# Optimization experiments

Measured on AMD Instinct MI355X. Metric: run time of the kernel, lower is better.

The kernel has to match this reference:

```python
import jax, jax.numpy as jnp
import numpy as np

B, C, H, W = 2, 64, 128, 128
K, SCALE, NUM_RES = 3, 2, 2
KK = K * K


def conv(x, w, b, pad=0):
    y = jax.lax.conv_general_dilated(x, w, (1, 1), [(pad, pad), (pad, pad)],
                                     dimension_numbers=('NCHW', 'OIHW', 'NCHW'))
    return y + b[None, :, None, None]


def unfold_dilated(x, k, d):
    # mimics nn.Unfold(kernel_size=k, dilation=d, padding=(k//2)*d) -> (b, c, k*k, h, w)
    pad = (k // 2) * d
    b, c, h, w = x.shape
    xp = jnp.pad(x, ((0, 0), (0, 0), (pad, pad), (pad, pad)))
    slices = [xp[:, :, i * d:i * d + h, j * d:j * d + w]
              for i in range(k) for j in range(k)]
    return jnp.stack(slices, axis=2)


def setup_inputs() -> dict:
    key = jax.random.key(0)
    ks = jax.random.split(key, 32)
    def p(k, shape, s=0.05):
        return jax.random.normal(k, shape, dtype=jnp.float32) * s
    H2, W2 = H * SCALE, W * SCALE
    return {
        'depth':  p(ks[0], (B, C, H2, W2), 1.0),
        'guide':  p(ks[1], (B, C, H2, W2), 1.0),
        'inputs': p(ks[2], (B, C, H, W), 1.0),
        # depth_kernel branch: 1x1 C->C (ReLU), 1x1 C->k^2
        'dk_w1': p(ks[3], (C, C, 1, 1)), 'dk_b1': jnp.zeros((C,), jnp.float32),
        'dk_w2': p(ks[4], (KK, C, 1, 1)), 'dk_b2': jnp.zeros((KK,), jnp.float32),
        # guide_kernel branch
        'gk_w1': p(ks[5], (C, C, 1, 1)), 'gk_b1': jnp.zeros((C,), jnp.float32),
        'gk_w2': p(ks[6], (KK, C, 1, 1)), 'gk_b2': jnp.zeros((KK,), jnp.float32),
        # weight_net: 3x3 2C->C (ReLU), 3x3 C->C (ReLU, TUnet stand-in), 3x3 C->1
        'wn_w1': p(ks[7], (C, 2 * C, 3, 3)), 'wn_b1': jnp.zeros((C,), jnp.float32),
        'wn_w2': p(ks[8], (C, C, 3, 3)), 'wn_b2': jnp.zeros((C,), jnp.float32),
        'wn_w3': p(ks[9], (1, C, 3, 3)), 'wn_b3': jnp.zeros((1,), jnp.float32),
        # residual blocks on inputs: NUM_RES x (conv3x3-ReLU-conv3x3 + skip)
        'rb_w': p(ks[10], (NUM_RES, 2, C, C, 3, 3)),
        'rb_b': jnp.zeros((NUM_RES, 2, C), jnp.float32),
        'aff_scale': 0.5 * KK * jnp.ones((1,), jnp.float32),
    }


def reference(depth, guide, inputs,
              dk_w1, dk_b1, dk_w2, dk_b2,
              gk_w1, gk_b1, gk_w2, gk_b2,
              wn_w1, wn_b1, wn_w2, wn_b2, wn_w3, wn_b3,
              rb_w, rb_b, aff_scale):
    # weight map
    wm = jax.nn.relu(conv(jnp.concatenate([depth, guide], axis=1), wn_w1, wn_b1, 1))
    wm = jax.nn.relu(conv(wm, wn_w2, wn_b2, 1))
    weight_map = conv(wm, wn_w3, wn_b3, 1)                       # (b,1,h_,w_)
    # per-pixel kernels
    dk = conv(jax.nn.relu(conv(depth, dk_w1, dk_b1)), dk_w2, dk_b2)
    gk = conv(jax.nn.relu(conv(guide, gk_w1, gk_b1)), gk_w2, gk_b2)
    dk = jax.nn.softmax(dk, axis=1)
    gk = jax.nn.softmax(gk, axis=1)
    fuse = weight_map * dk + (1.0 - weight_map) * gk
    fuse = jnp.tanh(fuse) / (aff_scale + 1e-8)
    ksum = jnp.maximum(jnp.sum(jnp.abs(fuse), axis=1, keepdims=True) + 1e-4, 1.0)
    fuse = fuse / ksum                                            # (b,k^2,h_,w_)
    # residual conv stack on low-res inputs
    x = inputs
    for i in range(NUM_RES):
        r = jax.nn.relu(conv(x, rb_w[i, 0], rb_b[i, 0], 1))
        r = conv(r, rb_w[i, 1], rb_b[i, 1], 1)
        x = x + r
    b, c, h, w = x.shape
    up = jax.image.resize(x, (b, c, h * SCALE, w * SCALE), method='bilinear')
    unf = unfold_dilated(up, K, SCALE)                            # (b,c,k^2,h_,w_)
    out = jnp.einsum('bkhw,bckhw->bchw', fuse, unf)
    return out
```

## Files before the change

### kernel.cpp

```cpp
#include <hip/hip_runtime.h>
#include <hip/hip_bf16.h>
#include <math.h>

#define HW2 (256*256)
#define HW1 (128*128)

typedef __attribute__((ext_vector_type(8))) short short8;
typedef __attribute__((ext_vector_type(4))) float floatx4;

__device__ __forceinline__ float b2f(ushort u) {
    union { unsigned int i; float f; } v; v.i = ((unsigned int)u) << 16; return v.f;
}
__device__ __forceinline__ ushort f2b(float f) {
    __hip_bfloat16 h = __float2bfloat16(f); return *(ushort*)&h;
}
__device__ __forceinline__ void pin(const short8& v) {
    asm volatile("" :: "v"(v));
}
__device__ __forceinline__ float fast_tanh(float x) {
    float cx = fminf(fmaxf(x, -15.f), 15.f);
    float t = __expf(2.f * cx);
    return (t - 1.f) / (t + 1.f);
}

__global__ __launch_bounds__(256)
void repack_all(const float* __restrict__ wn_w1, const float* __restrict__ wn_w2,
                const float* __restrict__ rb_w,
                const float* __restrict__ dk_w1, const float* __restrict__ gk_w1,
                const float* __restrict__ dk_w2, const float* __restrict__ gk_w2,
                const float* __restrict__ wn_w3,
                ushort* __restrict__ wt_wn1, ushort* __restrict__ wt_wn2,
                ushort* __restrict__ wt_rb,
                ushort* __restrict__ w1d, ushort* __restrict__ w1g,
                ushort* __restrict__ w2d, ushort* __restrict__ w2g,
                ushort* __restrict__ wt3) {
    int idx = blockIdx.x * 256 + threadIdx.x;
    int role = blockIdx.y;
    if (role == 0) {
        if (idx >= 73728) return;
        int o = idx / 1152; int rem = idx - o * 1152;
        int ci = rem / 9;   int t = rem - ci * 9;
        wt_wn1[(((size_t)(ci >> 5) * 9 + t) * 64 + o) * 32 + (ci & 31)] = f2b(wn_w1[idx]);
    } else if (role <= 5) {
        if (idx >= 36864) return;
        const float* w = (role == 1) ? wn_w2 : rb_w + (size_t)(role - 2) * 36864;
        ushort* wt     = (role == 1) ? wt_wn2 : wt_rb + (size_t)(role - 2) * 36864;
        int o = idx / 576; int rem = idx - o * 576;
        int ci = rem / 9;  int t = rem - ci * 9;
        wt[(((size_t)(ci >> 5) * 9 + t) * 64 + o) * 32 + (ci & 31)] = f2b(w[idx]);
    } else if (role == 6) {
        if (idx >= 10240) return;
        if (idx < 4096)      w1d[idx] = f2b(dk_w1[idx]);
        else if (idx < 8192) w1g[idx - 4096] = f2b(gk_w1[idx - 4096]);
        else if (idx < 9216) { int i = idx - 8192; w2d[i] = (i >> 6) < 9 ? f2b(dk_w2[i]) : (ushort)0; }
        else                 { int i = idx - 9216; w2g[i] = (i >> 6) < 9 ? f2b(gk_w2[i]) : (ushort)0; }
    } else {
        if (idx >= 9216) return;
        int kc = idx / 512; int rem = idx - kc * 512;
        int n = rem >> 5, c = rem & 31;
        int cc = kc / 9, t = kc - cc * 9;
        wt3[idx] = (n == 0) ? f2b(wn_w3[(cc * 32 + c) * 9 + t]) : (ushort)0;
    }
}

__global__ __launch_bounds__(256)
void to_chunked(const float* __restrict__ in, ushort* __restrict__ outc,
                int H, int W, int Cchunks) {
    int P = W + 2, Q = H + 2;
    int plane_px = P * Q;
    int idx = blockIdx.x * 256 + threadIdx.x;
    if (idx >= plane_px) return;
    int py = idx / P, px = idx - py * P;
    int bc = blockIdx.y;
    int b = bc / Cchunks, cc = bc - b * Cchunks;
    ushort* dst = outc + ((size_t)bc * plane_px + idx) * 32;
    if (py == 0 || py == Q - 1 || px == 0 || px == P - 1) {
        for (int c = 0; c < 32; ++c) dst[c] = 0;
        return;
    }
    int y = py - 1, x = px - 1;
    const float* src = in + ((size_t)b * (Cchunks * 32) + cc * 32) * H * W
                          + (size_t)y * W + x;
    for (int c = 0; c < 32; ++c)
        dst[c] = f2b(src[(size_t)c * H * W]);
}

__global__ __launch_bounds__(256)
void to_chunked_hi(const float* __restrict__ depth, const float* __restrict__ guide,
                   ushort* __restrict__ outc) {
    const int P = 258;
    int plane_px = P * P;
    int idx = blockIdx.x * 256 + threadIdx.x;
    if (idx >= plane_px) return;
    int py = idx / P, px = idx - py * P;
    int pl = blockIdx.y;
    const float* srcb = (pl < 4) ? depth : guide;
    int bc = pl & 3;
    int b = bc >> 1, cc = bc & 1;
    ushort* dst = outc + ((size_t)pl * plane_px + idx) * 32;
    if (py == 0 || py == P - 1 || px == 0 || px == P - 1) {
        for (int c = 0; c < 32; ++c) dst[c] = 0;
        return;
    }
    int y = py - 1, x = px - 1;
    const float* src = srcb + ((size_t)b * 64 + cc * 32) * HW2 + (size_t)y * 256 + x;
    for (int c = 0; c < 32; ++c)
        dst[c] = f2b(src[(size_t)c * HW2]);
}

__global__ __launch_bounds__(256)
void zero_border2(ushort* __restrict__ buf256, ushort* __restrict__ buf128) {
    int region = blockIdx.y;
    int H = region ? 128 : 256;
    int P = H + 2, Q = H + 2;
    ushort* buf = region ? buf128 : buf256;
    int nb = 2 * P + 2 * H;
    int idx = blockIdx.x * 256 + threadIdx.x;
    if (idx >= nb * 8) return;
    int pl = idx / nb, r = idx - pl * nb;
    int py, px;
    if (r < P)          { py = 0;     px = r; }
    else if (r < 2 * P) { py = Q - 1; px = r - P; }
    else { int k = r - 2 * P; py = 1 + (k >> 1); px = (k & 1) ? P - 1 : 0; }
    ushort* dst = buf + ((size_t)pl * P * Q + (size_t)py * P + px) * 32;
    for (int c = 0; c < 32; ++c) dst[c] = 0;
}

template<int NCHUNK, int ROWS, bool RELU, bool HAS_SKIP, bool CONCAT2>
__global__ __launch_bounds__(256)
void conv3x3_reg(const ushort* __restrict__ inA, const ushort* __restrict__ inB,
                 const ushort* __restrict__ wt, const float* __restrict__ bias,
                 const ushort* __restrict__ skip, ushort* __restrict__ outc,
                 int H, int W) {
    const int P = W + 2;
    const size_t plane = (size_t)P * (H + 2) * 32;
    int tid = threadIdx.x;
    int wv = tid >> 6, lane = tid & 63, ml = lane & 15, q = lane >> 4;
    int x0 = blockIdx.x * 16;
    int rowsPerBlock = (blockDim.x >> 6) * ROWS;
    int yb = blockIdx.y * rowsPerBlock + wv * ROWS;
    int b = blockIdx.z;

    floatx4 acc[ROWS][4];
#pragma unroll
    for (int r = 0; r < ROWS; ++r)
#pragma unroll
        for (int n = 0; n < 4; ++n) acc[r][n] = (floatx4){0.f, 0.f, 0.f, 0.f};

    for (int cc = 0; cc < NCHUNK; ++cc) {
        const ushort* base;
        if (CONCAT2) {
            constexpr int HC = NCHUNK / 2;
            if (cc < HC) base = inA + ((size_t)(b * HC + cc)) * plane;
            else         base = inB + ((size_t)(b * HC + cc - HC)) * plane;
        } else {
            base = inA + ((size_t)(b * NCHUNK + cc)) * plane;
        }
        const ushort* wb = wt + (size_t)cc * 18432;
#pragma unroll
        for (int t = 0; t < 9; ++t) {
            int dy = t / 3, dx = t - 3 * dy;
            short8 afr[ROWS], bfr[4];
#pragma unroll
            for (int r = 0; r < ROWS; ++r)
                afr[r] = *(const short8*)&base[((size_t)(yb + r + dy) * P
                                               + (x0 + ml + dx)) * 32 + q * 8];
#pragma unroll
            for (int n = 0; n < 4; ++n)
                bfr[n] = *(const short8*)&wb[(size_t)(t * 64 + n * 16 + ml) * 32 + q * 8];
#pragma unroll
            for (int r = 0; r < ROWS; ++r)
#pragma unroll
                for (int n = 0; n < 4; ++n)
                    acc[r][n] = __builtin_amdgcn_mfma_f32_16x16x32_bf16(
                        afr[r], bfr[n], acc[r][n], 0, 0, 0);
        }
    }

#pragma unroll
    for (int r = 0; r < ROWS; ++r) {
        int y = yb + r;
#pragma unroll
        for (int n = 0; n < 4; ++n) {
            int ch = n * 16 + ml;
            int occ = ch >> 5, ocl = ch & 31;
            float bs = bias[ch];
            size_t pbase = ((size_t)(b * 2 + occ)) * plane + ((size_t)(y + 1) * P) * 32 + ocl;
#pragma unroll
            for (int e = 0; e < 4; ++e) {
                int x = x0 + q * 4 + e;
                float v = acc[r][n][e] + bs;
                if (RELU) v = fmaxf(v, 0.f);
                if (HAS_SKIP)
                    v += b2f(skip[((size_t)(b * 2 + occ)) * plane
                                  + ((size_t)(y + 1) * P + (x + 1)) * 32 + ocl]);
                outc[pbase + (size_t)(x + 1) * 32] = f2b(v);
            }
        }
    }
}

__global__ __launch_bounds__(256, 2)
void kernels_fuse_mfma(const ushort* __restrict__ depth_c, const ushort* __restrict__ guide_c,
                       const ushort* __restrict__ bufB,
                       const ushort* __restrict__ wt3, const float* __restrict__ wn_b3,
                       const ushort* __restrict__ w1d, const float* __restrict__ b1d,
                       const ushort* __restrict__ w2d, const float* __restrict__ b2d,
                       const ushort* __restrict__ w1g, const float* __restrict__ b1g,
                       const ushort* __restrict__ w2g, const float* __restrict__ b2g,
                       const float* __restrict__ aff, float* __restrict__ fuse_out) {
    __shared__ __align__(16) ushort hid[2][4][16 * 72];
    __shared__ float wmv[4][16];

    int tid = threadIdx.x;
    int wv = tid >> 6, lane = tid & 63, ml = lane & 15, q = lane >> 4;
    int p0 = blockIdx.x * 64 + wv * 16;
    int b = p0 >> 16, rem0 = p0 & 65535;
    const size_t plane = (size_t)258 * 258 * 32;

    int rem = rem0 + ml;
    int y = rem >> 8, x = rem & 255;
    size_t poff = ((size_t)(y + 1) * 258 + (x + 1)) * 32;

    short8 afr[2][2];
#pragma unroll
    for (int kc = 0; kc < 2; ++kc) {
        afr[0][kc] = *(const short8*)&depth_c[(size_t)(b * 2 + kc) * plane + poff + q * 8];
        afr[1][kc] = *(const short8*)&guide_c[(size_t)(b * 2 + kc) * plane + poff + q * 8];
    }
    const ushort* bb0 = bufB + (size_t)(b * 2 + 0) * plane;
    const ushort* bb1 = bufB + (size_t)(b * 2 + 1) * plane;
    short8 a30[9], a31[9];
#pragma unroll
    for (int t = 0; t < 9; ++t) {
        int dy = t / 3, dx = t - 3 * dy;
        size_t o = ((size_t)(y + dy) * 258 + (x + dx)) * 32 + q * 8;
        a30[t] = *(const short8*)&bb0[o];
        a31[t] = *(const short8*)&bb1[o];
    }

    pin(afr[0][0]); pin(afr[0][1]); pin(afr[1][0]); pin(afr[1][1]);

    floatx4 acc[2][4];
#pragma unroll
    for (int br = 0; br < 2; ++br)
#pragma unroll
        for (int nt = 0; nt < 4; ++nt) acc[br][nt] = (floatx4){0.f, 0.f, 0.f, 0.f};
#pragma unroll
    for (int nt = 0; nt < 4; ++nt)
#pragma unroll
        for (int kc = 0; kc < 2; ++kc) {
            short8 bD = *(const short8*)&w1d[(size_t)((nt * 16 + ml) * 64 + kc * 32 + q * 8)];
            short8 bG = *(const short8*)&w1g[(size_t)((nt * 16 + ml) * 64 + kc * 32 + q * 8)];
            acc[0][nt] = __builtin_amdgcn_mfma_f32_16x16x32_bf16(afr[0][kc], bD, acc[0][nt], 0, 0, 0);
            acc[1][nt] = __builtin_amdgcn_mfma_f32_16x16x32_bf16(afr[1][kc], bG, acc[1][nt], 0, 0, 0);
        }

#pragma unroll
    for (int t = 0; t < 9; ++t) pin(a30[t]);
    floatx4 dw[4];
#pragma unroll
    for (int u = 0; u < 4; ++u) dw[u] = (floatx4){0.f, 0.f, 0.f, 0.f};
#pragma unroll
    for (int t = 0; t < 9; ++t) {
        short8 b3 = *(const short8*)&wt3[(size_t)(t * 512 + ml * 32 + q * 8)];
        dw[t & 3] = __builtin_amdgcn_mfma_f32_16x16x32_bf16(a30[t], b3, dw[t & 3], 0, 0, 0);
    }
#pragma unroll
    for (int t = 0; t < 9; ++t) pin(a31[t]);
#pragma unroll
    for (int t = 0; t < 9; ++t) {
        short8 b3 = *(const short8*)&wt3[(size_t)((9 + t) * 512 + ml * 32 + q * 8)];
        dw[t & 3] = __builtin_amdgcn_mfma_f32_16x16x32_bf16(a31[t], b3, dw[t & 3], 0, 0, 0);
    }
    floatx4 dwm = (dw[0] + dw[1]) + (dw[2] + dw[3]);
    if (ml == 0) {
#pragma unroll
        for (int e = 0; e < 4; ++e) wmv[wv][q * 4 + e] = dwm[e];
    }

#pragma unroll
    for (int br = 0; br < 2; ++br) {
        const float* b1 = br ? b1g : b1d;
        ushort* h = hid[br][wv];
#pragma unroll
        for (int nt = 0; nt < 4; ++nt) {
            float bs = b1[nt * 16 + ml];
#pragma unroll
            for (int e = 0; e < 4; ++e) {
                float v = acc[br][nt][e] + bs;
                v = fmaxf(v, 0.f);
                h[(q * 4 + e) * 72 + nt * 16 + ml] = f2b(v);
            }
        }
    }

    floatx4 d2[2];
    d2[0] = (floatx4){0.f, 0.f, 0.f, 0.f};
    d2[1] = (floatx4){0.f, 0.f, 0.f, 0.f};
#pragma unroll
    for (int kc = 0; kc < 2; ++kc) {
        short8 a2d = *(const short8*)&w2d[(size_t)(ml * 64 + kc * 32 + q * 8)];
        short8 a2g = *(const short8*)&w2g[(size_t)(ml * 64 + kc * 32 + q * 8)];
        short8 hfd = *(const short8*)&hid[0][wv][ml * 72 + kc * 32 + q * 8];
        short8 hfg = *(const short8*)&hid[1][wv][ml * 72 + kc * 32 + q * 8];
        d2[0] = __builtin_amdgcn_mfma_f32_16x16x32_bf16(a2d, hfd, d2[0], 0, 0, 0);
        d2[1] = __builtin_amdgcn_mfma_f32_16x16x32_bf16(a2g, hfg, d2[1], 0, 0, 0);
    }

    float wm = wmv[wv][ml] + wn_b3[0];

    float sm[2][4];
#pragma unroll
    for (int br = 0; br < 2; ++br) {
        const float* b2 = br ? b2g : b2d;
        float lg[4];
#pragma unroll
        for (int e = 0; e < 4; ++e) {
            int j = q * 4 + e;
            lg[e] = (j < 9) ? (d2[br][e] + b2[j]) : -1e30f;
        }
        float m = fmaxf(fmaxf(lg[0], lg[1]), fmaxf(lg[2], lg[3]));
        m = fmaxf(m, __shfl_xor(m, 16));
        m = fmaxf(m, __shfl_xor(m, 32));
        float s = 0.f;
#pragma unroll
        for (int e = 0; e < 4; ++e) { lg[e] = __expf(lg[e] - m); s += lg[e]; }
        s += __shfl_xor(s, 16);
        s += __shfl_xor(s, 32);
        float inv = 1.f / s;
#pragma unroll
        for (int e = 0; e < 4; ++e) sm[br][e] = lg[e] * inv;
    }

    float inv_av = 1.f / (aff[0] + 1e-8f);
    float f[4];
    float s = 0.f;
#pragma unroll
    for (int e = 0; e < 4; ++e) {
        float v = wm * sm[0][e] + (1.f - wm) * sm[1][e];
        v = fast_tanh(v) * inv_av;
        f[e] = v;
        s += fabsf(v);
    }
    s += __shfl_xor(s, 16);
    s += __shfl_xor(s, 32);
    float ksum = s + 1e-4f;
    if (ksum < 1.f) ksum = 1.f;
    float invk = 1.f / ksum;
#pragma unroll
    for (int e = 0; e < 4; ++e) {
        int j = q * 4 + e;
        if (j < 9)
            fuse_out[((size_t)b * 9 + j) * HW2 + rem0 + ml] = f[e] * invk;
    }
}

__global__ __launch_bounds__(256)
void fuse_apply_up(const float* __restrict__ fuse, const ushort* __restrict__ r2c,
                   float* __restrict__ out) {
    int p = blockIdx.x * 256 + threadIdx.x;
    int pl = blockIdx.y;
    int b = pl >> 1, cc = pl & 1;
    int y = p >> 8, x = p & 255;

    int my = y >> 1, mx = x >> 1;
    float wyA = (y & 1) ? 0.75f : 0.25f;  float wyB = 1.f - wyA;
    float wxA = (x & 1) ? 0.75f : 0.25f;  float wxB = 1.f - wxA;
    int R0y = my + ((y & 1) ? 0 : -1) - 1;
    int R0x = mx + ((x & 1) ? 0 : -1) - 1;

    const float* f = fuse + (size_t)b * 9 * HW2 + p;
    float coef[4][4];
#pragma unroll
    for (int k = 0; k < 4; ++k)
#pragma unroll
        for (int l = 0; l < 4; ++l) coef[k][l] = 0.f;

#pragma unroll
    for (int ty = 0; ty < 3; ++ty) {
        int yp = y + (ty - 1) * 2;
        if (yp < 0 || yp > 255) continue;
#pragma unroll
        for (int tx = 0; tx < 3; ++tx) {
            int xp = x + (tx - 1) * 2;
            if (xp < 0 || xp > 255) continue;
            float fv = f[(size_t)(ty * 3 + tx) * HW2];
            coef[ty][tx]         += fv * wyA * wxA;
            coef[ty][tx + 1]     += fv * wyA * wxB;
            coef[ty + 1][tx]     += fv * wyB * wxA;
            coef[ty + 1][tx + 1] += fv * wyB * wxB;
        }
    }

    const ushort* base = r2c + (size_t)pl * 130 * 130 * 32;
    float acc[32];
#pragma unroll
    for (int c = 0; c < 32; ++c) acc[c] = 0.f;
#pragma unroll
    for (int k = 0; k < 4; ++k) {
        int ry = R0y + k; ry = ry < 0 ? 0 : (ry > 127 ? 127 : ry);
#pragma unroll
        for (int l = 0; l < 4; ++l) {
            int rx = R0x + l; rx = rx < 0 ? 0 : (rx > 127 ? 127 : rx);
            float cf = coef[k][l];
            const ushort* u = base + ((size_t)(ry + 1) * 130 + (rx + 1)) * 32;
#pragma unroll
            for (int c = 0; c < 32; ++c) acc[c] = fmaf(cf, b2f(u[c]), acc[c]);
        }
    }
    float* ob = out + ((size_t)(b * 64 + cc * 32)) * HW2 + p;
#pragma unroll
    for (int c = 0; c < 32; ++c) ob[(size_t)c * HW2] = acc[c];
}

extern "C" void kernel_launch(void* const* d_in, const int* in_sizes, int n_in,
                              void* d_out, int out_size, void* d_ws, size_t ws_size,
                              hipStream_t stream) {
    const float* depth  = (const float*)d_in[0];
    const float* guide  = (const float*)d_in[1];
    const float* inputs = (const float*)d_in[2];
    const float* dk_w1  = (const float*)d_in[3];
    const float* dk_b1  = (const float*)d_in[4];
    const float* dk_w2  = (const float*)d_in[5];
    const float* dk_b2  = (const float*)d_in[6];
    const float* gk_w1  = (const float*)d_in[7];
    const float* gk_b1  = (const float*)d_in[8];
    const float* gk_w2  = (const float*)d_in[9];
    const float* gk_b2  = (const float*)d_in[10];
    const float* wn_w1  = (const float*)d_in[11];
    const float* wn_b1  = (const float*)d_in[12];
    const float* wn_w2  = (const float*)d_in[13];
    const float* wn_b2  = (const float*)d_in[14];
    const float* wn_w3  = (const float*)d_in[15];
    const float* wn_b3  = (const float*)d_in[16];
    const float* rb_w   = (const float*)d_in[17];
    const float* rb_b   = (const float*)d_in[18];
    const float* aff    = (const float*)d_in[19];
    float* out = (float*)d_out;

    float* ws = (float*)d_ws;
    size_t off = 0;
    const size_t CH256 = 4260096;
    const size_t CH128 = 1081600;
    ushort* depth_c = (ushort*)(ws + off); off += CH256;
    ushort* guide_c = (ushort*)(ws + off); off += CH256;
    ushort* bufA    = (ushort*)(ws + off); off += CH256;
    ushort* bufB    = (ushort*)(ws + off); off += CH256;
    ushort* inp_c   = (ushort*)(ws + off); off += CH128;
    ushort* r0      = (ushort*)(ws + off); off += CH128;
    ushort* r1      = (ushort*)(ws + off); off += CH128;
    ushort* r2      = (ushort*)(ws + off); off += CH128;
    float* fuse     = ws + off; off += 1179648;
    ushort* wt_wn1  = (ushort*)(ws + off); off += 36864;
    ushort* wt_wn2  = (ushort*)(ws + off); off += 18432;
    ushort* wt_rb   = (ushort*)(ws + off); off += 73728;
    ushort* w1d_b   = (ushort*)(ws + off); off += 2048;
    ushort* w1g_b   = (ushort*)(ws + off); off += 2048;
    ushort* w2d_b   = (ushort*)(ws + off); off += 512;
    ushort* w2g_b   = (ushort*)(ws + off); off += 512;
    ushort* wt3_b   = (ushort*)(ws + off); off += 4608;

    repack_all<<<dim3(288, 8), 256, 0, stream>>>(
        wn_w1, wn_w2, rb_w, dk_w1, gk_w1, dk_w2, gk_w2, wn_w3,
        wt_wn1, wt_wn2, wt_rb, w1d_b, w1g_b, w2d_b, w2g_b, wt3_b);

    to_chunked_hi<<<dim3(261, 8), 256, 0, stream>>>(depth, guide, depth_c);
    to_chunked<<<dim3(67, 4), 256, 0, stream>>>(inputs, inp_c, 128, 128, 2);

    zero_border2<<<dim3(33, 2), 256, 0, stream>>>(bufA, r0);

    conv3x3_reg<4, 4, true, false, true ><<<dim3(16, 16, 2), 256, 0, stream>>>(
        depth_c, guide_c, wt_wn1, wn_b1, nullptr, bufA, 256, 256);
    conv3x3_reg<2, 4, true, false, false><<<dim3(16, 16, 2), 256, 0, stream>>>(
        bufA, nullptr, wt_wn2, wn_b2, nullptr, bufB, 256, 256);

    kernels_fuse_mfma<<<2048, 256, 0, stream>>>(depth_c, guide_c, bufB,
                                                wt3_b, wn_b3,
                                                w1d_b, dk_b1, w2d_b, dk_b2,
                                                w1g_b, gk_b1, w2g_b, gk_b2,
                                                aff, fuse);

    conv3x3_reg<2, 2, true,  false, false><<<dim3(8, 16, 2), 256, 0, stream>>>(
        inp_c, nullptr, wt_rb + 0 * 36864, rb_b + 0 * 64, nullptr, r0, 128, 128);
    conv3x3_reg<2, 2, false, true,  false><<<dim3(8, 16, 2), 256, 0, stream>>>(
        r0, nullptr, wt_rb + 1 * 36864, rb_b + 1 * 64, inp_c, r1, 128, 128);
    conv3x3_reg<2, 2, true,  false, false><<<dim3(8, 16, 2), 256, 0, stream>>>(
        r1, nullptr, wt_rb + 2 * 36864, rb_b + 2 * 64, nullptr, r0, 128, 128);
    conv3x3_reg<2, 2, false, true,  false><<<dim3(8, 16, 2), 256, 0, stream>>>(
        r0, nullptr, wt_rb + 3 * 36864, rb_b + 3 * 64, r1, r2, 128, 128);

    fuse_apply_up<<<dim3(256, 4), 256, 0, stream>>>(fuse, r2, out);
}
```

Measured before the change: 334.9 us.

## Vectorize layout-conversion stores, batch conv loads per kernel row, drop register pins

The layout-conversion and border-zeroing kernels now write each pixel's 32 bf16 channels as four 16-byte vector stores instead of 32 scalar stores. The 3x3 conv loop is restructured to issue all A and B fragment loads for one kernel row (three taps) before the MFMAs, so more loads are in flight. The conv kernel also gets a launch-bounds occupancy hint of 2. The asm pin barriers in the fused kernel are removed, leaving load scheduling to the compiler. The trade-off is higher register pressure in the conv kernel and loss of the hand-forced load ordering.

```diff
diff --git a/kernel.cpp b/kernel.cpp
--- a/kernel.cpp
+++ b/kernel.cpp
@@ -13,9 +13,6 @@
 }
 __device__ __forceinline__ ushort f2b(float f) {
     __hip_bfloat16 h = __float2bfloat16(f); return *(ushort*)&h;
-}
-__device__ __forceinline__ void pin(const short8& v) {
-    asm volatile("" :: "v"(v));
 }
 __device__ __forceinline__ float fast_tanh(float x) {
     float cx = fminf(fmaxf(x, -15.f), 15.f);
@@ -74,15 +71,21 @@
     int bc = blockIdx.y;
     int b = bc / Cchunks, cc = bc - b * Cchunks;
     ushort* dst = outc + ((size_t)bc * plane_px + idx) * 32;
+    short8* d8 = (short8*)dst;
     if (py == 0 || py == Q - 1 || px == 0 || px == P - 1) {
-        for (int c = 0; c < 32; ++c) dst[c] = 0;
+        short8 z = (short8){0, 0, 0, 0, 0, 0, 0, 0};
+        d8[0] = z; d8[1] = z; d8[2] = z; d8[3] = z;
         return;
     }
     int y = py - 1, x = px - 1;
     const float* src = in + ((size_t)b * (Cchunks * 32) + cc * 32) * H * W
                           + (size_t)y * W + x;
+    ushort tmp[32];
+#pragma unroll
     for (int c = 0; c < 32; ++c)
-        dst[c] = f2b(src[(size_t)c * H * W]);
+        tmp[c] = f2b(src[(size_t)c * H * W]);
+#pragma unroll
+    for (int v = 0; v < 4; ++v) d8[v] = *(short8*)&tmp[v * 8];
 }
 
 __global__ __launch_bounds__(256)
@@ -98,14 +101,20 @@
     int bc = pl & 3;
     int b = bc >> 1, cc = bc & 1;
     ushort* dst = outc + ((size_t)pl * plane_px + idx) * 32;
+    short8* d8 = (short8*)dst;
     if (py == 0 || py == P - 1 || px == 0 || px == P - 1) {
-        for (int c = 0; c < 32; ++c) dst[c] = 0;
+        short8 z = (short8){0, 0, 0, 0, 0, 0, 0, 0};
+        d8[0] = z; d8[1] = z; d8[2] = z; d8[3] = z;
         return;
     }
     int y = py - 1, x = px - 1;
     const float* src = srcb + ((size_t)b * 64 + cc * 32) * HW2 + (size_t)y * 256 + x;
+    ushort tmp[32];
+#pragma unroll
     for (int c = 0; c < 32; ++c)
-        dst[c] = f2b(src[(size_t)c * HW2]);
+        tmp[c] = f2b(src[(size_t)c * HW2]);
+#pragma unroll
+    for (int v = 0; v < 4; ++v) d8[v] = *(short8*)&tmp[v * 8];
 }
 
 __global__ __launch_bounds__(256)
@@ -123,11 +132,13 @@
     else if (r < 2 * P) { py = Q - 1; px = r - P; }
     else { int k = r - 2 * P; py = 1 + (k >> 1); px = (k & 1) ? P - 1 : 0; }
     ushort* dst = buf + ((size_t)pl * P * Q + (size_t)py * P + px) * 32;
-    for (int c = 0; c < 32; ++c) dst[c] = 0;
+    short8 z = (short8){0, 0, 0, 0, 0, 0, 0, 0};
+    short8* d8 = (short8*)dst;
+    d8[0] = z; d8[1] = z; d8[2] = z; d8[3] = z;
 }
 
 template<int NCHUNK, int ROWS, bool RELU, bool HAS_SKIP, bool CONCAT2>
-__global__ __launch_bounds__(256)
+__global__ __launch_bounds__(256, 2)
 void conv3x3_reg(const ushort* __restrict__ inA, const ushort* __restrict__ inB,
                  const ushort* __restrict__ wt, const float* __restrict__ bias,
                  const ushort* __restrict__ skip, ushort* __restrict__ outc,
@@ -158,22 +169,27 @@
         }
         const ushort* wb = wt + (size_t)cc * 18432;
 #pragma unroll
-        for (int t = 0; t < 9; ++t) {
-            int dy = t / 3, dx = t - 3 * dy;
-            short8 afr[ROWS], bfr[4];
-#pragma unroll
-            for (int r = 0; r < ROWS; ++r)
-                afr[r] = *(const short8*)&base[((size_t)(yb + r + dy) * P
-                                               + (x0 + ml + dx)) * 32 + q * 8];
-#pragma unroll
-            for (int n = 0; n < 4; ++n)
-                bfr[n] = *(const short8*)&wb[(size_t)(t * 64 + n * 16 + ml) * 32 + q * 8];
-#pragma unroll
-            for (int r = 0; r < ROWS; ++r)
+        for (int dy = 0; dy < 3; ++dy) {
+            short8 afr[3][ROWS], bfr[3][4];
+#pragma unroll
+            for (int dx = 0; dx < 3; ++dx) {
+#pragma unroll
+                for (int r = 0; r < ROWS; ++r)
+                    afr[dx][r] = *(const short8*)&base[((size_t)(yb + r + dy) * P
+                                                       + (x0 + ml + dx)) * 32 + q * 8];
 #pragma unroll
                 for (int n = 0; n < 4; ++n)
-                    acc[r][n] = __builtin_amdgcn_mfma_f32_16x16x32_bf16(
-                        afr[r], bfr[n], acc[r][n], 0, 0, 0);
+                    bfr[dx][n] = *(const short8*)&wb[(size_t)((dy * 3 + dx) * 64
+                                                              + n * 16 + ml) * 32 + q * 8];
+            }
+#pragma unroll
+            for (int dx = 0; dx < 3; ++dx)
+#pragma unroll
+                for (int r = 0; r < ROWS; ++r)
+#pragma unroll
+                    for (int n = 0; n < 4; ++n)
+                        acc[r][n] = __builtin_amdgcn_mfma_f32_16x16x32_bf16(
+                            afr[dx][r], bfr[dx][n], acc[r][n], 0, 0, 0);
         }
     }
 
@@ -239,8 +255,6 @@
         a31[t] = *(const short8*)&bb1[o];
     }
 
-    pin(afr[0][0]); pin(afr[0][1]); pin(afr[1][0]); pin(afr[1][1]);
-
     floatx4 acc[2][4];
 #pragma unroll
     for (int br = 0; br < 2; ++br)
@@ -256,8 +270,6 @@
             acc[1][nt] = __builtin_amdgcn_mfma_f32_16x16x32_bf16(afr[1][kc], bG, acc[1][nt], 0, 0, 0);
         }
 
-#pragma unroll
-    for (int t = 0; t < 9; ++t) pin(a30[t]);
     floatx4 dw[4];
 #pragma unroll
     for (int u = 0; u < 4; ++u) dw[u] = (floatx4){0.f, 0.f, 0.f, 0.f};
@@ -266,8 +278,6 @@
         short8 b3 = *(const short8*)&wt3[(size_t)(t * 512 + ml * 32 + q * 8)];
         dw[t & 3] = __builtin_amdgcn_mfma_f32_16x16x32_bf16(a30[t], b3, dw[t & 3], 0, 0, 0);
     }
-#pragma unroll
-    for (int t = 0; t < 9; ++t) pin(a31[t]);
 #pragma unroll
     for (int t = 0; t < 9; ++t) {
         short8 b3 = *(const short8*)&wt3[(size_t)((9 + t) * 512 + ml * 32 + q * 8)];
```

Result: no change. 329.8 us (-1.5%).
